# Performance work log

Hardware: AMD Instinct MI355X
Metric: run time of the kernel (lower is better)

The kernel has to match this reference:

```python
import jax, jax.numpy as jnp
import numpy as np

B, N, C, H = 8, 1024, 1024, 16
D = C // H
SCALE = D ** -0.5

def setup_inputs() -> dict:
    key = jax.random.key(0)
    k1, k2, k3, k4 = jax.random.split(key, 4)
    x = jax.random.normal(k1, (B, N, C), dtype=jnp.float32)
    # qkv: Linear(dim, 3*dim, bias=False); stored as [C, 3C] for x @ W
    w_qkv = jax.random.normal(k2, (C, 3 * C), dtype=jnp.float32) * (C ** -0.5)
    # proj: Linear(out_dim=C, dim=C) with bias
    w_proj = jax.random.normal(k3, (C, C), dtype=jnp.float32) * (C ** -0.5)
    b_proj = jax.random.normal(k4, (C,), dtype=jnp.float32) * 0.01
    return {"x": x, "w_qkv": w_qkv, "w_proj": w_proj, "b_proj": b_proj}

def reference(x, w_qkv, w_proj, b_proj):
    b, n, c = x.shape
    qkv = (x @ w_qkv).reshape(b, n, 3, H, D)
    qkv = jnp.transpose(qkv, (2, 0, 3, 1, 4))  # [3, B, H, N, D]
    q, k, v = qkv[0], qkv[1], qkv[2]
    # standard QK attention
    attn_ori = jax.nn.softmax(jnp.einsum('bhnd,bhmd->bhnm', q, k) * SCALE, axis=-1)
    # dual VV self-attention (k = v; q = k)
    attn = jax.nn.softmax(jnp.einsum('bhnd,bhmd->bhnm', v, v) * SCALE, axis=-1)
    x_ori = jnp.einsum('bhnm,bhmd->bhnd', attn_ori, v)
    x_new = jnp.einsum('bhnm,bhmd->bhnd', attn, v)
    x_ori = jnp.transpose(x_ori, (0, 2, 1, 3)).reshape(b, n, c)
    x_new = jnp.transpose(x_new, (0, 2, 1, 3)).reshape(b, n, c)
    out = x_new @ w_proj + b_proj
    out_ori = x_ori @ w_proj + b_proj
    return out, out_ori
```

## Files before the change

### kernel.cpp

```cpp
#include <hip/hip_runtime.h>
#include <hip/hip_bf16.h>

#define BATCH 8
#define NSEQ  1024
#define CDIM  1024
#define NHEAD 16
#define HDIM  64
#define QKSCALE 0.125f

typedef __bf16 bf16;
typedef bf16  bf16x8 __attribute__((ext_vector_type(8)));
typedef bf16  bf16x4 __attribute__((ext_vector_type(4)));
typedef bf16  bf16x2 __attribute__((ext_vector_type(2)));
typedef float f32x4  __attribute__((ext_vector_type(4)));
typedef float f32x16 __attribute__((ext_vector_type(16)));
typedef unsigned u32x4 __attribute__((ext_vector_type(4)));

#if __has_builtin(__builtin_amdgcn_permlane32_swap)
static __device__ inline void plswap(unsigned &a, unsigned &b) {
    typedef unsigned u32x2v __attribute__((ext_vector_type(2)));
    u32x2v r = __builtin_amdgcn_permlane32_swap(a, b, false, false);
    a = r[0]; b = r[1];
}
#else
static __device__ inline void plswap(unsigned &a, unsigned &b) {
    asm volatile("v_permlane32_swap_b32 %0, %1" : "+v"(a), "+v"(b));
}
#endif

__global__ __launch_bounds__(256) void k_cvt_x(const float* __restrict__ x,
                                               bf16* __restrict__ xb) {
    int i = blockIdx.x * 256 + threadIdx.x;
    float4 v = reinterpret_cast<const float4*>(x)[i];
    bf16x4 o = { (bf16)v.x, (bf16)v.y, (bf16)v.z, (bf16)v.w };
    reinterpret_cast<bf16x4*>(xb)[i] = o;
}

__global__ __launch_bounds__(256) void k_transpose(const float* __restrict__ w,
                                                   bf16* __restrict__ wt,
                                                   int R, int C) {
    __shared__ bf16 tile[32][33];
    int c0 = blockIdx.x * 32, r0 = blockIdx.y * 32;
    int tx = threadIdx.x & 31, ty = threadIdx.x >> 5;
    #pragma unroll
    for (int rr = ty; rr < 32; rr += 8)
        tile[rr][tx] = (bf16)w[(size_t)(r0 + rr) * C + c0 + tx];
    __syncthreads();
    #pragma unroll
    for (int cc = ty; cc < 32; cc += 8)
        wt[(size_t)(c0 + cc) * R + r0 + tx] = tile[tx][cc];
}

__global__ __launch_bounds__(256) void k_ktile(const bf16* __restrict__ src,
                                               bf16* __restrict__ dst) {
    const int tid = threadIdx.x, wv = tid >> 6, l = tid & 63;
    const int col = l & 31, hi = l >> 5;
    const int head = blockIdx.y;
    const int kvblk = blockIdx.x * 4 + wv;
    const bf16* s = src + (size_t)head * NSEQ * HDIM
                        + (size_t)(kvblk * 32 + col) * HDIM + hi * 8;
    bf16* d = dst + (size_t)head * 65536 + (size_t)kvblk * 2048 + (size_t)l * 8;
    #pragma unroll
    for (int dblk = 0; dblk < 4; ++dblk)
        *reinterpret_cast<bf16x8*>(d + dblk * 512) =
            *reinterpret_cast<const bf16x8*>(s + dblk * 16);
}

__global__ __launch_bounds__(256) void k_vtile(const bf16* __restrict__ src,
                                               bf16* __restrict__ dst) {
    const int tid = threadIdx.x, wv = tid >> 6, l = tid & 63;
    const int col = l & 31, hi = l >> 5;
    const int head = blockIdx.y;
    const int kvb = blockIdx.x * 4 + wv;
    const bf16* s = src + (size_t)head * NSEQ * HDIM;
    bf16* d = dst + (size_t)head * 65536 + (size_t)kvb * 1024 + (size_t)l * 8;
    #pragma unroll
    for (int dt = 0; dt < 2; ++dt) {
        bf16x8 v;
        #pragma unroll
        for (int j = 0; j < 8; ++j)
            v[j] = s[(size_t)(kvb * 16 + hi * 8 + j) * HDIM + dt * 32 + col];
        *reinterpret_cast<bf16x8*>(d + dt * 512) = v;
    }
}

template <int EPI>
__global__ __launch_bounds__(256) void k_gemm(
    const bf16* __restrict__ A, const bf16* __restrict__ Bt,
    int K, int Ncols,
    float* __restrict__ out, const float* __restrict__ bias,
    bf16* __restrict__ qb, bf16* __restrict__ kb,
    bf16* __restrict__ vb) {
    __shared__ __align__(16) bf16 As[128 * 32];
    __shared__ __align__(16) bf16 Bs[128 * 32];
    const int tid = threadIdx.x;
    const int wv = tid >> 6, l = tid & 63, lr = l & 15, lg = l >> 4;
    const int wr = wv >> 1, wc = wv & 1;
    const int bm = blockIdx.x, bn = blockIdx.y;
    f32x4 acc[4][4] = {};
    const bf16* Abase = A + (size_t)(bm * 128) * K;
    const bf16* Bbase = Bt + (size_t)(bn * 128) * K;

    for (int k0 = 0; k0 < K; k0 += 32) {
        #pragma unroll
        for (int i = 0; i < 2; ++i) {
            int e = (i * 256 + tid) * 8;
            int r = e >> 5, c = e & 31;
            __builtin_amdgcn_global_load_lds(
                (const __attribute__((address_space(1))) unsigned int*)(Abase + (size_t)r * K + k0 + c),
                (__attribute__((address_space(3))) unsigned int*)(As + e), 16, 0, 0);
            __builtin_amdgcn_global_load_lds(
                (const __attribute__((address_space(1))) unsigned int*)(Bbase + (size_t)r * K + k0 + c),
                (__attribute__((address_space(3))) unsigned int*)(Bs + e), 16, 0, 0);
        }
        asm volatile("s_waitcnt vmcnt(0)" ::: "memory");
        __syncthreads();
        bf16x8 af[4], bfr[4];
        #pragma unroll
        for (int m = 0; m < 4; ++m)
            af[m] = *reinterpret_cast<const bf16x8*>(As + (wr * 64 + m * 16 + lr) * 32 + lg * 8);
        #pragma unroll
        for (int n = 0; n < 4; ++n)
            bfr[n] = *reinterpret_cast<const bf16x8*>(Bs + (wc * 64 + n * 16 + lr) * 32 + lg * 8);
        #pragma unroll
        for (int m = 0; m < 4; ++m)
            #pragma unroll
            for (int n = 0; n < 4; ++n)
                acc[m][n] = __builtin_amdgcn_mfma_f32_16x16x32_bf16(af[m], bfr[n], acc[m][n], 0, 0, 0);
        __syncthreads();
    }

    #pragma unroll
    for (int m = 0; m < 4; ++m) {
        #pragma unroll
        for (int n = 0; n < 4; ++n) {
            #pragma unroll
            for (int r = 0; r < 4; ++r) {
                int gr = bm * 128 + wr * 64 + m * 16 + lg * 4 + r;
                int gc = bn * 128 + wc * 64 + n * 16 + lr;
                float val = acc[m][n][r];
                if (EPI == 0) {
                    int b = gr >> 10, nn = gr & 1023;
                    int t = gc >> 10, hc = gc & 1023;
                    int h = hc >> 6, d = hc & 63;
                    size_t idx = (((size_t)(b * NHEAD + h)) * NSEQ + nn) * HDIM + d;
                    bf16 bvv = (bf16)val;
                    if (t == 0) qb[idx] = bvv;
                    else if (t == 1) kb[idx] = bvv;
                    else vb[idx] = bvv;
                } else {
                    out[(size_t)gr * Ncols + gc] = val + bias[gc];
                }
            }
        }
    }
}

__global__ __launch_bounds__(256) void k_attn2(const bf16* __restrict__ qb,
                                               const bf16* __restrict__ vb,
                                               const bf16* __restrict__ ktK,
                                               const bf16* __restrict__ ktV,
                                               const bf16* __restrict__ vtile,
                                               bf16* __restrict__ xo,
                                               bf16* __restrict__ xn) {
    const int tid = threadIdx.x, wv = tid >> 6, l = tid & 63;
    const int col = l & 31, hi = l >> 5;

    const int lid = blockIdx.x;
    const int xcd = lid & 7, j = lid >> 3;
    const int head = xcd * 16 + (j >> 4);
    const int inner = j & 15;
    const int which = inner >> 3;
    const int qtile = inner & 7;

    const int b = head >> 4, h = head & 15;
    const int q0 = qtile * 128 + wv * 32;
    const bf16* Qrow = (which ? vb : qb) + (size_t)head * NSEQ * HDIM;
    const bf16* Kt = (which ? ktV : ktK) + (size_t)head * 65536;
    const bf16* Vt = vtile + (size_t)head * 65536;
    bf16* Out = which ? xn : xo;

    bf16x8 bqf[4];
    {
        const bf16* qp = Qrow + (size_t)(q0 + col) * HDIM + hi * 8;
        #pragma unroll
        for (int dblk = 0; dblk < 4; ++dblk)
            bqf[dblk] = *reinterpret_cast<const bf16x8*>(qp + dblk * 16);
    }
    f32x16 o0 = {}, o1 = {};
    float l_ = 0.f;

    for (int kv = 0; kv < NSEQ; kv += 32) {
        const int kvblk = kv >> 5;
        bf16x8 akf[4];
        {
            const bf16* kp = Kt + (size_t)kvblk * 2048 + (size_t)l * 8;
            #pragma unroll
            for (int dblk = 0; dblk < 4; ++dblk)
                akf[dblk] = *reinterpret_cast<const bf16x8*>(kp + dblk * 512);
        }
        bf16x8 bvf[2][2];
        {
            const bf16* vp = Vt + (size_t)(kv >> 4) * 1024 + (size_t)l * 8;
            #pragma unroll
            for (int kb2 = 0; kb2 < 2; ++kb2)
                #pragma unroll
                for (int dt = 0; dt < 2; ++dt)
                    bvf[dt][kb2] = *reinterpret_cast<const bf16x8*>(vp + kb2 * 1024 + dt * 512);
        }
        f32x16 st = {};
        __builtin_amdgcn_s_setprio(1);
        #pragma unroll
        for (int dblk = 0; dblk < 4; ++dblk)
            st = __builtin_amdgcn_mfma_f32_32x32x16_bf16(akf[dblk], bqf[dblk], st, 0, 0, 0);
        __builtin_amdgcn_s_setprio(0);
        float rs = 0.f;
        unsigned pk0, pk1, pk2, pk3, pk4, pk5, pk6, pk7;
        {
            float p[16];
            #pragma unroll
            for (int r = 0; r < 16; ++r) {
                p[r] = __expf(st[r] * QKSCALE);
                rs += p[r];
            }
            bf16x2 t0 = { (bf16)p[0],  (bf16)p[1]  }; pk0 = __builtin_bit_cast(unsigned, t0);
            bf16x2 t1 = { (bf16)p[2],  (bf16)p[3]  }; pk1 = __builtin_bit_cast(unsigned, t1);
            bf16x2 t2 = { (bf16)p[4],  (bf16)p[5]  }; pk2 = __builtin_bit_cast(unsigned, t2);
            bf16x2 t3 = { (bf16)p[6],  (bf16)p[7]  }; pk3 = __builtin_bit_cast(unsigned, t3);
            bf16x2 t4 = { (bf16)p[8],  (bf16)p[9]  }; pk4 = __builtin_bit_cast(unsigned, t4);
            bf16x2 t5 = { (bf16)p[10], (bf16)p[11] }; pk5 = __builtin_bit_cast(unsigned, t5);
            bf16x2 t6 = { (bf16)p[12], (bf16)p[13] }; pk6 = __builtin_bit_cast(unsigned, t6);
            bf16x2 t7 = { (bf16)p[14], (bf16)p[15] }; pk7 = __builtin_bit_cast(unsigned, t7);
        }
        l_ += rs;
        unsigned f0a = pk0, f0c = pk2; plswap(f0a, f0c);
        unsigned f0b = pk1, f0d = pk3; plswap(f0b, f0d);
        unsigned f1a = pk4, f1c = pk6; plswap(f1a, f1c);
        unsigned f1b = pk5, f1d = pk7; plswap(f1b, f1d);
        u32x4 w0 = { f0a, f0b, f0c, f0d };
        u32x4 w1 = { f1a, f1b, f1c, f1d };
        bf16x8 pf0 = __builtin_bit_cast(bf16x8, w0);
        bf16x8 pf1 = __builtin_bit_cast(bf16x8, w1);
        __builtin_amdgcn_s_setprio(1);
        o0 = __builtin_amdgcn_mfma_f32_32x32x16_bf16(pf0, bvf[0][0], o0, 0, 0, 0);
        o0 = __builtin_amdgcn_mfma_f32_32x32x16_bf16(pf1, bvf[0][1], o0, 0, 0, 0);
        o1 = __builtin_amdgcn_mfma_f32_32x32x16_bf16(pf0, bvf[1][0], o1, 0, 0, 0);
        o1 = __builtin_amdgcn_mfma_f32_32x32x16_bf16(pf1, bvf[1][1], o1, 0, 0, 0);
        __builtin_amdgcn_s_setprio(0);
    }
    float lt = l_ + __shfl_xor(l_, 32);
    float inv = 1.f / lt;
    bf16* orow = Out + ((size_t)b * NSEQ + q0) * CDIM + h * HDIM;
    #pragma unroll
    for (int r = 0; r < 16; ++r) {
        int q = (r & 3) + 8 * (r >> 2) + 4 * hi;
        float iv = __shfl(inv, q);
        orow[(size_t)q * CDIM + col]      = (bf16)(o0[r] * iv);
        orow[(size_t)q * CDIM + 32 + col] = (bf16)(o1[r] * iv);
    }
}

extern "C" void kernel_launch(void* const* d_in, const int* in_sizes, int n_in,
                              void* d_out, int out_size, void* d_ws, size_t ws_size,
                              hipStream_t stream) {
    const float* x      = (const float*)d_in[0];
    const float* w_qkv  = (const float*)d_in[1];
    const float* w_proj = (const float*)d_in[2];
    const float* b_proj = (const float*)d_in[3];
    float* out = (float*)d_out;

    char* ws = (char*)d_ws;
    size_t off = 0;
    const size_t SZ_X   = (size_t)BATCH * NSEQ * CDIM * 2;
    const size_t SZ_QKV = (size_t)BATCH * NHEAD * NSEQ * HDIM * 2;
    bf16* xb    = (bf16*)(ws + off); off += SZ_X;
    bf16* wqkvT = (bf16*)(ws + off); off += (size_t)3 * CDIM * CDIM * 2;
    bf16* wpT   = (bf16*)(ws + off); off += (size_t)CDIM * CDIM * 2;
    bf16* qb    = (bf16*)(ws + off); off += SZ_QKV;
    bf16* kb    = (bf16*)(ws + off); off += SZ_QKV;
    bf16* vb    = (bf16*)(ws + off); off += SZ_QKV;
    bf16* ktK   = (bf16*)(ws + off); off += SZ_QKV;
    bf16* ktV   = (bf16*)(ws + off); off += SZ_QKV;
    bf16* vtile = (bf16*)(ws + off); off += SZ_QKV;
    bf16* xn    = (bf16*)(ws + off); off += SZ_X;
    bf16* xo    = (bf16*)(ws + off); off += SZ_X;

    k_cvt_x<<<dim3((BATCH * NSEQ * CDIM) / (256 * 4)), 256, 0, stream>>>(x, xb);
    k_transpose<<<dim3(3 * CDIM / 32, CDIM / 32), 256, 0, stream>>>(w_qkv, wqkvT, CDIM, 3 * CDIM);
    k_transpose<<<dim3(CDIM / 32, CDIM / 32), 256, 0, stream>>>(w_proj, wpT, CDIM, CDIM);

    k_gemm<0><<<dim3((BATCH * NSEQ) / 128, (3 * CDIM) / 128), 256, 0, stream>>>(
        xb, wqkvT, CDIM, 3 * CDIM, nullptr, nullptr, qb, kb, vb);

    k_ktile<<<dim3(NSEQ / 128, BATCH * NHEAD), 256, 0, stream>>>(kb, ktK);
    k_ktile<<<dim3(NSEQ / 128, BATCH * NHEAD), 256, 0, stream>>>(vb, ktV);
    k_vtile<<<dim3(NSEQ / 64, BATCH * NHEAD), 256, 0, stream>>>(vb, vtile);

    k_attn2<<<dim3(2048), 256, 0, stream>>>(qb, vb, ktK, ktV, vtile, xo, xn);

    k_gemm<1><<<dim3((2 * BATCH * NSEQ) / 128, CDIM / 128), 256, 0, stream>>>(
        xn, wpT, CDIM, CDIM, out, b_proj, nullptr, nullptr, nullptr);
}
```

Before: 356.0 us.

## Fuse K/V tiling into QKV GEMM epilogue, add grid swizzle, use exp2

The QKV GEMM epilogue now writes K and V straight into the tiled layouts the attention kernel reads, so the three separate ktile/vtile relayout kernels and the intermediate K buffer go away. Both GEMMs switch to a 1D grid with an XCD-aware, grouped tile remap meant to improve L2 reuse across the chiplets. Softmax exponentials use a hardware exp2 with a folded log2(e)*scale constant. The epilogue now does scattered 2-byte stores to three V destinations, which could cost write efficiency.

```diff
diff --git a/kernel.cpp b/kernel.cpp
--- a/kernel.cpp
+++ b/kernel.cpp
@@ -7,6 +7,7 @@
 #define NHEAD 16
 #define HDIM  64
 #define QKSCALE 0.125f
+#define QKC     0.18033688011112042f
 
 typedef __bf16 bf16;
 typedef bf16  bf16x8 __attribute__((ext_vector_type(8)));
@@ -28,6 +29,14 @@
 }
 #endif
 
+static __device__ inline float fast_exp2(float x) {
+#if __has_builtin(__builtin_amdgcn_exp2f)
+    return __builtin_amdgcn_exp2f(x);
+#else
+    return __expf(x * 0.6931471805599453f);
+#endif
+}
+
 __global__ __launch_bounds__(256) void k_cvt_x(const float* __restrict__ x,
                                                bf16* __restrict__ xb) {
     int i = blockIdx.x * 256 + threadIdx.x;
@@ -51,52 +60,23 @@
         wt[(size_t)(c0 + cc) * R + r0 + tx] = tile[tx][cc];
 }
 
-__global__ __launch_bounds__(256) void k_ktile(const bf16* __restrict__ src,
-                                               bf16* __restrict__ dst) {
-    const int tid = threadIdx.x, wv = tid >> 6, l = tid & 63;
-    const int col = l & 31, hi = l >> 5;
-    const int head = blockIdx.y;
-    const int kvblk = blockIdx.x * 4 + wv;
-    const bf16* s = src + (size_t)head * NSEQ * HDIM
-                        + (size_t)(kvblk * 32 + col) * HDIM + hi * 8;
-    bf16* d = dst + (size_t)head * 65536 + (size_t)kvblk * 2048 + (size_t)l * 8;
-    #pragma unroll
-    for (int dblk = 0; dblk < 4; ++dblk)
-        *reinterpret_cast<bf16x8*>(d + dblk * 512) =
-            *reinterpret_cast<const bf16x8*>(s + dblk * 16);
-}
-
-__global__ __launch_bounds__(256) void k_vtile(const bf16* __restrict__ src,
-                                               bf16* __restrict__ dst) {
-    const int tid = threadIdx.x, wv = tid >> 6, l = tid & 63;
-    const int col = l & 31, hi = l >> 5;
-    const int head = blockIdx.y;
-    const int kvb = blockIdx.x * 4 + wv;
-    const bf16* s = src + (size_t)head * NSEQ * HDIM;
-    bf16* d = dst + (size_t)head * 65536 + (size_t)kvb * 1024 + (size_t)l * 8;
-    #pragma unroll
-    for (int dt = 0; dt < 2; ++dt) {
-        bf16x8 v;
-        #pragma unroll
-        for (int j = 0; j < 8; ++j)
-            v[j] = s[(size_t)(kvb * 16 + hi * 8 + j) * HDIM + dt * 32 + col];
-        *reinterpret_cast<bf16x8*>(d + dt * 512) = v;
-    }
-}
-
 template <int EPI>
 __global__ __launch_bounds__(256) void k_gemm(
     const bf16* __restrict__ A, const bf16* __restrict__ Bt,
-    int K, int Ncols,
+    int K, int Ncols, int nbn,
     float* __restrict__ out, const float* __restrict__ bias,
-    bf16* __restrict__ qb, bf16* __restrict__ kb,
-    bf16* __restrict__ vb) {
+    bf16* __restrict__ qb, bf16* __restrict__ vbp,
+    bf16* __restrict__ ktK, bf16* __restrict__ ktV,
+    bf16* __restrict__ vtile) {
     __shared__ __align__(16) bf16 As[128 * 32];
     __shared__ __align__(16) bf16 Bs[128 * 32];
     const int tid = threadIdx.x;
     const int wv = tid >> 6, l = tid & 63, lr = l & 15, lg = l >> 4;
     const int wr = wv >> 1, wc = wv & 1;
-    const int bm = blockIdx.x, bn = blockIdx.y;
+    const int nwg = gridDim.x;
+    const int w = (blockIdx.x & 7) * (nwg >> 3) + (blockIdx.x >> 3);
+    const int sup = w / (8 * nbn), t0 = w % (8 * nbn);
+    const int bm = sup * 8 + (t0 & 7), bn = t0 >> 3;
     f32x4 acc[4][4] = {};
     const bf16* Abase = A + (size_t)(bm * 128) * K;
     const bf16* Bbase = Bt + (size_t)(bn * 128) * K;
@@ -143,11 +123,24 @@
                     int b = gr >> 10, nn = gr & 1023;
                     int t = gc >> 10, hc = gc & 1023;
                     int h = hc >> 6, d = hc & 63;
-                    size_t idx = (((size_t)(b * NHEAD + h)) * NSEQ + nn) * HDIM + d;
+                    int head = b * NHEAD + h;
                     bf16 bvv = (bf16)val;
-                    if (t == 0) qb[idx] = bvv;
-                    else if (t == 1) kb[idx] = bvv;
-                    else vb[idx] = bvv;
+                    if (t == 0) {
+                        qb[((size_t)head * NSEQ + nn) * HDIM + d] = bvv;
+                    } else {
+                        size_t kaddr = (size_t)head * 65536
+                                     + (size_t)(nn >> 5) * 2048 + (size_t)(d >> 4) * 512
+                                     + (size_t)((((d >> 3) & 1) << 5) + (nn & 31)) * 8 + (d & 7);
+                        if (t == 1) {
+                            ktK[kaddr] = bvv;
+                        } else {
+                            ktV[kaddr] = bvv;
+                            vbp[((size_t)head * NSEQ + nn) * HDIM + d] = bvv;
+                            vtile[(size_t)head * 65536
+                                  + (size_t)(nn >> 4) * 1024 + (size_t)(d >> 5) * 512
+                                  + (size_t)((((nn >> 3) & 1) << 5) + (d & 31)) * 8 + (nn & 7)] = bvv;
+                        }
+                    }
                 } else {
                     out[(size_t)gr * Ncols + gc] = val + bias[gc];
                 }
@@ -220,7 +213,7 @@
             float p[16];
             #pragma unroll
             for (int r = 0; r < 16; ++r) {
-                p[r] = __expf(st[r] * QKSCALE);
+                p[r] = fast_exp2(st[r] * QKC);
                 rs += p[r];
             }
             bf16x2 t0 = { (bf16)p[0],  (bf16)p[1]  }; pk0 = __builtin_bit_cast(unsigned, t0);
@@ -277,7 +270,6 @@
     bf16* wqkvT = (bf16*)(ws + off); off += (size_t)3 * CDIM * CDIM * 2;
     bf16* wpT   = (bf16*)(ws + off); off += (size_t)CDIM * CDIM * 2;
     bf16* qb    = (bf16*)(ws + off); off += SZ_QKV;
-    bf16* kb    = (bf16*)(ws + off); off += SZ_QKV;
     bf16* vb    = (bf16*)(ws + off); off += SZ_QKV;
     bf16* ktK   = (bf16*)(ws + off); off += SZ_QKV;
     bf16* ktV   = (bf16*)(ws + off); off += SZ_QKV;
@@ -289,15 +281,11 @@
     k_transpose<<<dim3(3 * CDIM / 32, CDIM / 32), 256, 0, stream>>>(w_qkv, wqkvT, CDIM, 3 * CDIM);
     k_transpose<<<dim3(CDIM / 32, CDIM / 32), 256, 0, stream>>>(w_proj, wpT, CDIM, CDIM);
 
-    k_gemm<0><<<dim3((BATCH * NSEQ) / 128, (3 * CDIM) / 128), 256, 0, stream>>>(
-        xb, wqkvT, CDIM, 3 * CDIM, nullptr, nullptr, qb, kb, vb);
-
-    k_ktile<<<dim3(NSEQ / 128, BATCH * NHEAD), 256, 0, stream>>>(kb, ktK);
-    k_ktile<<<dim3(NSEQ / 128, BATCH * NHEAD), 256, 0, stream>>>(vb, ktV);
-    k_vtile<<<dim3(NSEQ / 64, BATCH * NHEAD), 256, 0, stream>>>(vb, vtile);
+    k_gemm<0><<<dim3(64 * 24), 256, 0, stream>>>(
+        xb, wqkvT, CDIM, 3 * CDIM, 24, nullptr, nullptr, qb, vb, ktK, ktV, vtile);
 
     k_attn2<<<dim3(2048), 256, 0, stream>>>(qb, vb, ktK, ktV, vtile, xo, xn);
 
-    k_gemm<1><<<dim3((2 * BATCH * NSEQ) / 128, CDIM / 128), 256, 0, stream>>>(
-        xn, wpT, CDIM, CDIM, out, b_proj, nullptr, nullptr, nullptr);
-}
+    k_gemm<1><<<dim3(128 * 8), 256, 0, stream>>>(
+        xn, wpT, CDIM, CDIM, 8, out, b_proj, nullptr, nullptr, nullptr, nullptr, nullptr);
+}
```

New measurement: 344.6 us. 1.03x faster.
